# Kernel tuning notes

Hardware: AMD Instinct MI355X
Metric: run time of the kernel (lower is better)

The kernel has to match this reference:

```python
import jax, jax.numpy as jnp
import numpy as np

WIN = (4, 4, 4)   # (wd, wh, ww), window seq len s = 64
HEADS = 4


def setup_inputs() -> dict:
    key = jax.random.key(0)
    k1, k2, k3 = jax.random.split(key, 3)
    B, D, H, W, C = 1, 32, 64, 128, 96
    x = jax.random.normal(k1, (B, D, H, W, C), dtype=jnp.float32)
    # weights stored in (in, out) layout; math identical to torch Linear (x @ W.T)
    w_qkv = jax.random.normal(k2, (C, 3 * C), dtype=jnp.float32) * (C ** -0.5)
    w_proj = jax.random.normal(k3, (C, C), dtype=jnp.float32) * (C ** -0.5)
    b_proj = jnp.zeros((C,), dtype=jnp.float32)
    return {"x": x, "w_qkv": w_qkv, "w_proj": w_proj, "b_proj": b_proj}


def reference(x, w_qkv, w_proj, b_proj):
    B, D, H, W, C = x.shape
    wd, wh, ww = WIN
    h = HEADS
    ch = C // h
    s = wd * wh * ww
    scale = ch ** -0.5
    n, m, l = D // wd, H // wh, W // ww
    # window partition: [B,D,H,W,C] -> [B,n,m,l,s,C]
    xw = x.reshape(B, n, wd, m, wh, l, ww, C)
    xw = xw.transpose(0, 1, 3, 5, 2, 4, 6, 7).reshape(B, n, m, l, s, C)
    # QKV projection (no bias)
    qkv = xw @ w_qkv                      # [B,n,m,l,s,3C]
    q, k, v = jnp.split(qkv, 3, axis=-1)  # each [B,n,m,l,s,C]

    def to_heads(t):
        return t.reshape(B, n, m, l, s, h, ch).transpose(0, 1, 2, 3, 5, 4, 6)

    q, k, v = to_heads(q), to_heads(k), to_heads(v)  # [B,n,m,l,h,s,ch]
    attn = jnp.einsum('bnmlhsc,bnmlhtc->bnmlhst', q, k) * scale
    attn = jax.nn.softmax(attn, axis=-1)             # [B,n,m,l,h,s,s]
    out = jnp.einsum('bnmlhst,bnmlhtc->bnmlhsc', attn, v)
    # merge heads: [B,n,m,l,h,s,ch] -> [B,n,m,l,s,C]
    out = out.transpose(0, 1, 2, 3, 5, 4, 6).reshape(B, n, m, l, s, C)
    out = out @ w_proj + b_proj
    # window merge back to [B,D,H,W,C]
    out = out.reshape(B, n, m, l, wd, wh, ww, C)
    out = out.transpose(0, 1, 4, 2, 5, 3, 6, 7).reshape(B, D, H, W, C)
    return out
```

## Files before the change

kernel.cpp:

```cpp
#include <hip/hip_runtime.h>
#include <hip/hip_bf16.h>

typedef __attribute__((ext_vector_type(8))) short bf16x8;
typedef __attribute__((ext_vector_type(4))) float f32x4;
typedef __attribute__((ext_vector_type(4))) unsigned short u16x4;
typedef __attribute__((ext_vector_type(4))) unsigned int u32x4;
typedef __attribute__((ext_vector_type(2))) unsigned int u32x2;

#define MFMA16(a, b, c) __builtin_amdgcn_mfma_f32_16x16x32_bf16((a), (b), (c), 0, 0, 0)

#define WQT_ELEMS 27648
#define WPT_ELEMS 9216

__device__ __forceinline__ unsigned short cvt_bf(float f) {
    __hip_bfloat16 h = __float2bfloat16(f);
    return *reinterpret_cast<unsigned short*>(&h);
}
__device__ __forceinline__ unsigned pack2bf(float a, float b) {
    return (unsigned)cvt_bf(a) | ((unsigned)cvt_bf(b) << 16);
}

__global__ void wconv_kernel(const float* __restrict__ wqkv,
                             const float* __restrict__ wproj,
                             unsigned short* __restrict__ wsT) {
    int o = blockIdx.x * 256 + threadIdx.x;
    if (o < WQT_ELEMS) {
        int j = o / 96, c = o % 96;
        float w = wqkv[c * 288 + j];
        if (j < 96) w *= 0.2944889313f;
        wsT[o] = cvt_bf(w);
    } else if (o < WQT_ELEMS + WPT_ELEMS) {
        int o2 = o - WQT_ELEMS;
        int j = o2 / 96, c = o2 % 96;
        wsT[o] = cvt_bf(wproj[c * 96 + j]);
    }
}

__device__ __forceinline__ int xq_addr(int t, int c) {
    return ((c >> 5) << 12) + ((t >> 1) << 7)
         + ((((t & 1) << 6) + ((c & 31) << 1)) ^ (((t >> 1) & 7) << 4));
}

#define LOADW(m, W0, W1, W2) do {                                              \
    const unsigned short* _wp = wsT + ((m) * 16 + p) * 96 + qg * 8;            \
    W0 = *reinterpret_cast<const bf16x8*>(_wp);                                \
    W1 = *reinterpret_cast<const bf16x8*>(_wp + 32);                           \
    W2 = *reinterpret_cast<const bf16x8*>(_wp + 64);                           \
} while (0)

#define MFMA_T(W0, W1, W2)                                                     \
    f32x4 ac0 = fzero, ac1 = fzero, ac2 = fzero, ac3 = fzero;                  \
    ac0 = MFMA16(W0, a00, ac0); ac1 = MFMA16(W0, a10, ac1);                    \
    ac2 = MFMA16(W0, a20, ac2); ac3 = MFMA16(W0, a30, ac3);                    \
    ac0 = MFMA16(W1, a01, ac0); ac1 = MFMA16(W1, a11, ac1);                    \
    ac2 = MFMA16(W1, a21, ac2); ac3 = MFMA16(W1, a31, ac3);                    \
    ac0 = MFMA16(W2, a02, ac0); ac1 = MFMA16(W2, a12, ac1);                    \
    ac2 = MFMA16(W2, a22, ac2); ac3 = MFMA16(W2, a32, ac3);

#define DO_Q(m, W0, W1, W2) do {                                               \
    MFMA_T(W0, W1, W2)                                                         \
    int ch = (m) * 16 + 4 * qg;                                                \
    *reinterpret_cast<u32x2*>(xq + xq_addr(p,      ch)) = (u32x2){pack2bf(ac0[0],ac0[1]), pack2bf(ac0[2],ac0[3])}; \
    *reinterpret_cast<u32x2*>(xq + xq_addr(16 + p, ch)) = (u32x2){pack2bf(ac1[0],ac1[1]), pack2bf(ac1[2],ac1[3])}; \
    *reinterpret_cast<u32x2*>(xq + xq_addr(32 + p, ch)) = (u32x2){pack2bf(ac2[0],ac2[1]), pack2bf(ac2[2],ac2[3])}; \
    *reinterpret_cast<u32x2*>(xq + xq_addr(48 + p, ch)) = (u32x2){pack2bf(ac3[0],ac3[1]), pack2bf(ac3[2],ac3[3])}; \
} while (0)

#define DO_K(m, W0, W1, W2) do {                                               \
    MFMA_T(W0, W1, W2)                                                         \
    int jk = ((m) - 6) * 16 + 4 * qg;                                          \
    int cb = jk * 2 + (jk / 24) * 16;                                          \
    int sw = (p & 7) << 4;                                                     \
    *reinterpret_cast<u32x2*>(ksb + (p)      * 256 + (cb ^ sw)) = (u32x2){pack2bf(ac0[0],ac0[1]), pack2bf(ac0[2],ac0[3])}; \
    *reinterpret_cast<u32x2*>(ksb + (16 + p) * 256 + (cb ^ sw)) = (u32x2){pack2bf(ac1[0],ac1[1]), pack2bf(ac1[2],ac1[3])}; \
    *reinterpret_cast<u32x2*>(ksb + (32 + p) * 256 + (cb ^ sw)) = (u32x2){pack2bf(ac2[0],ac2[1]), pack2bf(ac2[2],ac2[3])}; \
    *reinterpret_cast<u32x2*>(ksb + (48 + p) * 256 + (cb ^ sw)) = (u32x2){pack2bf(ac3[0],ac3[1]), pack2bf(ac3[2],ac3[3])}; \
} while (0)

#define STV1(JV, A, T2) do {                                                   \
    int _r0 = (JV);                                                            \
    *reinterpret_cast<unsigned short*>(vtb + (_r0)     * 128 + ((T2) ^ (((_r0)     & 7) << 4))) = cvt_bf(A[0]); \
    *reinterpret_cast<unsigned short*>(vtb + (_r0 + 1) * 128 + ((T2) ^ (((_r0 + 1) & 7) << 4))) = cvt_bf(A[1]); \
    *reinterpret_cast<unsigned short*>(vtb + (_r0 + 2) * 128 + ((T2) ^ (((_r0 + 2) & 7) << 4))) = cvt_bf(A[2]); \
    *reinterpret_cast<unsigned short*>(vtb + (_r0 + 3) * 128 + ((T2) ^ (((_r0 + 3) & 7) << 4))) = cvt_bf(A[3]); \
} while (0)

#define DO_V(m, W0, W1, W2) do {                                               \
    MFMA_T(W0, W1, W2)                                                         \
    int jv = ((m) - 12) * 16 + 4 * qg;                                         \
    STV1(jv, ac0, (p) * 2);                                                    \
    STV1(jv, ac1, (16 + p) * 2);                                               \
    STV1(jv, ac2, (32 + p) * 2);                                               \
    STV1(jv, ac3, (48 + p) * 2);                                               \
} while (0)

#define LOADWP(m, W0, W1, W2) do {                                             \
    const unsigned short* _wp = wpT + ((m) * 16 + p) * 96 + qg * 8;            \
    W0 = *reinterpret_cast<const bf16x8*>(_wp);                                \
    W1 = *reinterpret_cast<const bf16x8*>(_wp + 32);                           \
    W2 = *reinterpret_cast<const bf16x8*>(_wp + 64);                           \
} while (0)

#define PROJ(m, W0, W1, W2) do {                                               \
    f32x4 acc = fzero;                                                         \
    acc = MFMA16(W0, o0, acc);                                                 \
    acc = MFMA16(W1, o1, acc);                                                 \
    acc = MFMA16(W2, o2, acc);                                                 \
    float4 bb = *reinterpret_cast<const float4*>(bproj + (m) * 16 + 4 * qg);   \
    f32x4 r;                                                                   \
    r[0] = acc[0] + bb.x; r[1] = acc[1] + bb.y;                                \
    r[2] = acc[2] + bb.z; r[3] = acc[3] + bb.w;                                \
    *reinterpret_cast<f32x4*>(fbuf + (wv * 16 + p) * 100 + (m) * 16 + 4 * qg) = r; \
} while (0)

__global__ __launch_bounds__(256, 3)
void winattn_kernel(const float* __restrict__ x,
                    const unsigned short* __restrict__ wsT,
                    const float* __restrict__ bproj,
                    float* __restrict__ out) {
    __shared__ __align__(16) char LDS[40960];
    char* xq  = LDS;
    char* ksb = LDS + 12288;
    char* vtb = LDS + 28672;
    float* fbuf = reinterpret_cast<float*>(LDS + 12288);

    const int tid = threadIdx.x;
    const int lane = tid & 63;
    const int wv = tid >> 6;
    const int p  = lane & 15;
    const int qg = lane >> 4;

    const int iw  = blockIdx.x;
    const int l_i = iw & 31;
    const int m_i = (iw >> 5) & 15;
    const int n_i = iw >> 9;

    const f32x4 fzero = {0.f, 0.f, 0.f, 0.f};

    bf16x8 wA0, wA1, wA2, wB0, wB1, wB2;
    const int tb0 = (wv < 2) ? wv * 5 : 10 + (wv - 2) * 4;
    LOADW(tb0, wA0, wA1, wA2);

    #pragma unroll
    for (int it = 0; it < 6; ++it) {
        int slot = tid + it * 256;
        int t = slot / 24, cq = slot % 24;
        int td = t >> 4, th = (t >> 2) & 3, tw = t & 3;
        int off = (((n_i * 4 + td) * 64 + (m_i * 4 + th)) * 128 + (l_i * 4 + tw)) * 96 + cq * 4;
        float4 v4 = *reinterpret_cast<const float4*>(x + off);
        u16x4 h;
        h[0] = cvt_bf(v4.x); h[1] = cvt_bf(v4.y); h[2] = cvt_bf(v4.z); h[3] = cvt_bf(v4.w);
        *reinterpret_cast<u16x4*>(xq + xq_addr(t, cq * 4)) = h;
    }
    {
        int t = tid >> 2, hd = tid & 3;
        bf16x8 z = {0, 0, 0, 0, 0, 0, 0, 0};
        int cb = hd * 64 + 48;
        *reinterpret_cast<bf16x8*>(ksb + t * 256 + (cb ^ ((t & 7) << 4))) = z;
    }
    __syncthreads();

    bf16x8 a00, a01, a02, a10, a11, a12, a20, a21, a22, a30, a31, a32;
    {
        const char* xb = xq;
        a00 = *reinterpret_cast<const bf16x8*>(xb + xq_addr(p,      qg * 8));
        a01 = *reinterpret_cast<const bf16x8*>(xb + xq_addr(p,      32 + qg * 8));
        a02 = *reinterpret_cast<const bf16x8*>(xb + xq_addr(p,      64 + qg * 8));
        a10 = *reinterpret_cast<const bf16x8*>(xb + xq_addr(16 + p, qg * 8));
        a11 = *reinterpret_cast<const bf16x8*>(xb + xq_addr(16 + p, 32 + qg * 8));
        a12 = *reinterpret_cast<const bf16x8*>(xb + xq_addr(16 + p, 64 + qg * 8));
        a20 = *reinterpret_cast<const bf16x8*>(xb + xq_addr(32 + p, qg * 8));
        a21 = *reinterpret_cast<const bf16x8*>(xb + xq_addr(32 + p, 32 + qg * 8));
        a22 = *reinterpret_cast<const bf16x8*>(xb + xq_addr(32 + p, 64 + qg * 8));
        a30 = *reinterpret_cast<const bf16x8*>(xb + xq_addr(48 + p, qg * 8));
        a31 = *reinterpret_cast<const bf16x8*>(xb + xq_addr(48 + p, 32 + qg * 8));
        a32 = *reinterpret_cast<const bf16x8*>(xb + xq_addr(48 + p, 64 + qg * 8));
    }
    __syncthreads();

    if (wv == 0) {
        LOADW(1, wB0, wB1, wB2); DO_Q(0, wA0, wA1, wA2);
        LOADW(2, wA0, wA1, wA2); DO_Q(1, wB0, wB1, wB2);
        LOADW(3, wB0, wB1, wB2); DO_Q(2, wA0, wA1, wA2);
        LOADW(4, wA0, wA1, wA2); DO_Q(3, wB0, wB1, wB2);
        DO_Q(4, wA0, wA1, wA2);
    } else if (wv == 1) {
        LOADW(6, wB0, wB1, wB2); DO_Q(5, wA0, wA1, wA2);
        LOADW(7, wA0, wA1, wA2); DO_K(6, wB0, wB1, wB2);
        LOADW(8, wB0, wB1, wB2); DO_K(7, wA0, wA1, wA2);
        LOADW(9, wA0, wA1, wA2); DO_K(8, wB0, wB1, wB2);
        DO_K(9, wA0, wA1, wA2);
    } else if (wv == 2) {
        LOADW(11, wB0, wB1, wB2); DO_K(10, wA0, wA1, wA2);
        LOADW(12, wA0, wA1, wA2); DO_K(11, wB0, wB1, wB2);
        LOADW(13, wB0, wB1, wB2); DO_V(12, wA0, wA1, wA2);
        DO_V(13, wB0, wB1, wB2);
    } else {
        LOADW(15, wB0, wB1, wB2); DO_V(14, wA0, wA1, wA2);
        LOADW(16, wA0, wA1, wA2); DO_V(15, wB0, wB1, wB2);
        LOADW(17, wB0, wB1, wB2); DO_V(16, wA0, wA1, wA2);
        DO_V(17, wB0, wB1, wB2);
    }
    __syncthreads();

    #pragma unroll 1
    for (int hd = 0; hd < 4; ++hd) {
        bf16x8 aqh = *reinterpret_cast<const bf16x8*>(xq + xq_addr(wv * 16 + p, hd * 24 + qg * 8));
        f32x4 sacc[4];
        #pragma unroll
        for (int nt = 0; nt < 4; ++nt) {
            int t = nt * 16 + p;
            bf16x8 ak = *reinterpret_cast<const bf16x8*>(ksb + t * 256 + ((hd * 64 + qg * 16) ^ ((t & 7) << 4)));
            sacc[nt] = MFMA16(ak, aqh, fzero);
        }
        float mm = sacc[0][0];
        #pragma unroll
        for (int nt = 0; nt < 4; ++nt)
            #pragma unroll
            for (int rg = 0; rg < 4; ++rg)
                mm = fmaxf(mm, sacc[nt][rg]);
        mm = fmaxf(mm, __shfl_xor(mm, 16));
        mm = fmaxf(mm, __shfl_xor(mm, 32));
        float pw[4][4];
        float sum = 0.f;
        #pragma unroll
        for (int nt = 0; nt < 4; ++nt)
            #pragma unroll
            for (int rg = 0; rg < 4; ++rg) {
                float e = exp2f(sacc[nt][rg] - mm);
                pw[nt][rg] = e;
                sum += e;
            }
        sum += __shfl_xor(sum, 16);
        sum += __shfl_xor(sum, 32);
        float inv = 1.0f / sum;
        unsigned pk[4][2];
        #pragma unroll
        for (int nt = 0; nt < 4; ++nt) {
            pk[nt][0] = pack2bf(pw[nt][0] * inv, pw[nt][1] * inv);
            pk[nt][1] = pack2bf(pw[nt][2] * inv, pw[nt][3] * inv);
        }
        u32x4 pa0, pa1;
        #pragma unroll
        for (int d = 0; d < 4; ++d) {
            int src = ((qg & 1) * 2 + (d >> 1)) * 16 + p;
            int lo0 = __shfl((int)pk[0][d & 1], src);
            int hi0 = __shfl((int)pk[1][d & 1], src);
            int lo1 = __shfl((int)pk[2][d & 1], src);
            int hi1 = __shfl((int)pk[3][d & 1], src);
            pa0[d] = (qg < 2) ? (unsigned)lo0 : (unsigned)hi0;
            pa1[d] = (qg < 2) ? (unsigned)lo1 : (unsigned)hi1;
        }
        bf16x8 pA0 = __builtin_bit_cast(bf16x8, pa0);
        bf16x8 pA1 = __builtin_bit_cast(bf16x8, pa1);
        f32x4 oacc[2] = {fzero, fzero};
        #pragma unroll
        for (int n2 = 0; n2 < 2; ++n2) {
            int vr = hd * 24 + n2 * 16 + p;
            vr = vr > 95 ? 95 : vr;
            int rb = vr * 128, sw = (vr & 7) << 4;
            bf16x8 av0 = *reinterpret_cast<const bf16x8*>(vtb + rb + ((qg * 16) ^ sw));
            bf16x8 av1 = *reinterpret_cast<const bf16x8*>(vtb + rb + ((64 + qg * 16) ^ sw));
            oacc[n2] = MFMA16(av0, pA0, oacc[n2]);
            oacc[n2] = MFMA16(av1, pA1, oacc[n2]);
        }
        {
            u32x2 w0 = { pack2bf(oacc[0][0], oacc[0][1]), pack2bf(oacc[0][2], oacc[0][3]) };
            *reinterpret_cast<u32x2*>(xq + xq_addr(wv * 16 + p, hd * 24 + 4 * qg)) = w0;
            if (qg < 2) {
                u32x2 w1 = { pack2bf(oacc[1][0], oacc[1][1]), pack2bf(oacc[1][2], oacc[1][3]) };
                *reinterpret_cast<u32x2*>(xq + xq_addr(wv * 16 + p, hd * 24 + 16 + 4 * qg)) = w1;
            }
        }
    }

    bf16x8 o0, o1, o2;
    o0 = *reinterpret_cast<const bf16x8*>(xq + xq_addr(wv * 16 + p, qg * 8));
    o1 = *reinterpret_cast<const bf16x8*>(xq + xq_addr(wv * 16 + p, 32 + qg * 8));
    o2 = *reinterpret_cast<const bf16x8*>(xq + xq_addr(wv * 16 + p, 64 + qg * 8));
    __syncthreads();

    const unsigned short* wpT = wsT + WQT_ELEMS;
    LOADWP(0, wA0, wA1, wA2);
    LOADWP(1, wB0, wB1, wB2); PROJ(0, wA0, wA1, wA2);
    LOADWP(2, wA0, wA1, wA2); PROJ(1, wB0, wB1, wB2);
    LOADWP(3, wB0, wB1, wB2); PROJ(2, wA0, wA1, wA2);
    LOADWP(4, wA0, wA1, wA2); PROJ(3, wB0, wB1, wB2);
    LOADWP(5, wB0, wB1, wB2); PROJ(4, wA0, wA1, wA2);
    PROJ(5, wB0, wB1, wB2);
    __syncthreads();

    #pragma unroll
    for (int it = 0; it < 6; ++it) {
        int slot = tid + it * 256;
        int t = slot / 24, cq = slot % 24;
        int td = t >> 4, th = (t >> 2) & 3, tw = t & 3;
        int off = (((n_i * 4 + td) * 64 + (m_i * 4 + th)) * 128 + (l_i * 4 + tw)) * 96 + cq * 4;
        float4 v4 = *reinterpret_cast<const float4*>(fbuf + t * 100 + cq * 4);
        *reinterpret_cast<float4*>(out + off) = v4;
    }
}

extern "C" void kernel_launch(void* const* d_in, const int* in_sizes, int n_in,
                              void* d_out, int out_size, void* d_ws, size_t ws_size,
                              hipStream_t stream) {
    const float* x     = (const float*)d_in[0];
    const float* wqkv  = (const float*)d_in[1];
    const float* wproj = (const float*)d_in[2];
    const float* bproj = (const float*)d_in[3];
    float* out = (float*)d_out;
    unsigned short* wsT = (unsigned short*)d_ws;

    wconv_kernel<<<dim3((WQT_ELEMS + WPT_ELEMS) / 256), dim3(256), 0, stream>>>(wqkv, wproj, wsT);
    winattn_kernel<<<dim3(4096), dim3(256), 0, stream>>>(x, wsT, bproj, out);
}
```

Before: 80.16 us.

## Store K in compact xq layout, shrink LDS, raise occupancy to four blocks

K is now written into the same compact 96-channel swizzled layout as Q instead of a padded 256-byte-per-row layout with zeroed head padding. Padding lanes are handled by zeroing the Q operand for qg==3 and clamping the read column, so the per-block zero-fill pass goes away. fbuf is moved to alias the start of LDS. Together these cut LDS from 40 KB to 36 KB, and launch bounds go from 3 to 4 blocks per CU to allow more resident waves. The risks are register pressure under the tighter launch bound and a correctness hazard if fbuf overwrites Q or K before every wave has finished reading them.

```diff
diff --git a/kernel.cpp b/kernel.cpp
--- a/kernel.cpp
+++ b/kernel.cpp
@@ -57,25 +57,16 @@
     ac0 = MFMA16(W2, a02, ac0); ac1 = MFMA16(W2, a12, ac1);                    \
     ac2 = MFMA16(W2, a22, ac2); ac3 = MFMA16(W2, a32, ac3);
 
-#define DO_Q(m, W0, W1, W2) do {                                               \
+#define DO_QK(DST, ch, W0, W1, W2) do {                                        \
     MFMA_T(W0, W1, W2)                                                         \
-    int ch = (m) * 16 + 4 * qg;                                                \
-    *reinterpret_cast<u32x2*>(xq + xq_addr(p,      ch)) = (u32x2){pack2bf(ac0[0],ac0[1]), pack2bf(ac0[2],ac0[3])}; \
-    *reinterpret_cast<u32x2*>(xq + xq_addr(16 + p, ch)) = (u32x2){pack2bf(ac1[0],ac1[1]), pack2bf(ac1[2],ac1[3])}; \
-    *reinterpret_cast<u32x2*>(xq + xq_addr(32 + p, ch)) = (u32x2){pack2bf(ac2[0],ac2[1]), pack2bf(ac2[2],ac2[3])}; \
-    *reinterpret_cast<u32x2*>(xq + xq_addr(48 + p, ch)) = (u32x2){pack2bf(ac3[0],ac3[1]), pack2bf(ac3[2],ac3[3])}; \
-} while (0)
-
-#define DO_K(m, W0, W1, W2) do {                                               \
-    MFMA_T(W0, W1, W2)                                                         \
-    int jk = ((m) - 6) * 16 + 4 * qg;                                          \
-    int cb = jk * 2 + (jk / 24) * 16;                                          \
-    int sw = (p & 7) << 4;                                                     \
-    *reinterpret_cast<u32x2*>(ksb + (p)      * 256 + (cb ^ sw)) = (u32x2){pack2bf(ac0[0],ac0[1]), pack2bf(ac0[2],ac0[3])}; \
-    *reinterpret_cast<u32x2*>(ksb + (16 + p) * 256 + (cb ^ sw)) = (u32x2){pack2bf(ac1[0],ac1[1]), pack2bf(ac1[2],ac1[3])}; \
-    *reinterpret_cast<u32x2*>(ksb + (32 + p) * 256 + (cb ^ sw)) = (u32x2){pack2bf(ac2[0],ac2[1]), pack2bf(ac2[2],ac2[3])}; \
-    *reinterpret_cast<u32x2*>(ksb + (48 + p) * 256 + (cb ^ sw)) = (u32x2){pack2bf(ac3[0],ac3[1]), pack2bf(ac3[2],ac3[3])}; \
-} while (0)
+    *reinterpret_cast<u32x2*>((DST) + xq_addr(p,      (ch))) = (u32x2){pack2bf(ac0[0],ac0[1]), pack2bf(ac0[2],ac0[3])}; \
+    *reinterpret_cast<u32x2*>((DST) + xq_addr(16 + p, (ch))) = (u32x2){pack2bf(ac1[0],ac1[1]), pack2bf(ac1[2],ac1[3])}; \
+    *reinterpret_cast<u32x2*>((DST) + xq_addr(32 + p, (ch))) = (u32x2){pack2bf(ac2[0],ac2[1]), pack2bf(ac2[2],ac2[3])}; \
+    *reinterpret_cast<u32x2*>((DST) + xq_addr(48 + p, (ch))) = (u32x2){pack2bf(ac3[0],ac3[1]), pack2bf(ac3[2],ac3[3])}; \
+} while (0)
+
+#define DO_Q(m, W0, W1, W2) DO_QK(xq, (m) * 16 + 4 * qg, W0, W1, W2)
+#define DO_K(m, W0, W1, W2) DO_QK(kb, ((m) - 6) * 16 + 4 * qg, W0, W1, W2)
 
 #define STV1(JV, A, T2) do {                                                   \
     int _r0 = (JV);                                                            \
@@ -113,16 +104,16 @@
     *reinterpret_cast<f32x4*>(fbuf + (wv * 16 + p) * 100 + (m) * 16 + 4 * qg) = r; \
 } while (0)
 
-__global__ __launch_bounds__(256, 3)
+__global__ __launch_bounds__(256, 4)
 void winattn_kernel(const float* __restrict__ x,
                     const unsigned short* __restrict__ wsT,
                     const float* __restrict__ bproj,
                     float* __restrict__ out) {
-    __shared__ __align__(16) char LDS[40960];
+    __shared__ __align__(16) char LDS[36864];
     char* xq  = LDS;
-    char* ksb = LDS + 12288;
-    char* vtb = LDS + 28672;
-    float* fbuf = reinterpret_cast<float*>(LDS + 12288);
+    char* kb  = LDS + 12288;
+    char* vtb = LDS + 24576;
+    float* fbuf = reinterpret_cast<float*>(LDS);
 
     const int tid = threadIdx.x;
     const int lane = tid & 63;
@@ -136,6 +127,7 @@
     const int n_i = iw >> 9;
 
     const f32x4 fzero = {0.f, 0.f, 0.f, 0.f};
+    const bf16x8 zero8 = {0, 0, 0, 0, 0, 0, 0, 0};
 
     bf16x8 wA0, wA1, wA2, wB0, wB1, wB2;
     const int tb0 = (wv < 2) ? wv * 5 : 10 + (wv - 2) * 4;
@@ -151,12 +143,6 @@
         u16x4 h;
         h[0] = cvt_bf(v4.x); h[1] = cvt_bf(v4.y); h[2] = cvt_bf(v4.z); h[3] = cvt_bf(v4.w);
         *reinterpret_cast<u16x4*>(xq + xq_addr(t, cq * 4)) = h;
-    }
-    {
-        int t = tid >> 2, hd = tid & 3;
-        bf16x8 z = {0, 0, 0, 0, 0, 0, 0, 0};
-        int cb = hd * 64 + 48;
-        *reinterpret_cast<bf16x8*>(ksb + t * 256 + (cb ^ ((t & 7) << 4))) = z;
     }
     __syncthreads();
 
@@ -205,12 +191,14 @@
 
     #pragma unroll 1
     for (int hd = 0; hd < 4; ++hd) {
-        bf16x8 aqh = *reinterpret_cast<const bf16x8*>(xq + xq_addr(wv * 16 + p, hd * 24 + qg * 8));
+        int qc = hd * 24 + qg * 8;
+        qc = qc > 88 ? 88 : qc;
+        bf16x8 aq_raw = *reinterpret_cast<const bf16x8*>(xq + xq_addr(wv * 16 + p, qc));
+        bf16x8 aqh = (qg == 3) ? zero8 : aq_raw;
         f32x4 sacc[4];
         #pragma unroll
         for (int nt = 0; nt < 4; ++nt) {
-            int t = nt * 16 + p;
-            bf16x8 ak = *reinterpret_cast<const bf16x8*>(ksb + t * 256 + ((hd * 64 + qg * 16) ^ ((t & 7) << 4)));
+            bf16x8 ak = *reinterpret_cast<const bf16x8*>(kb + xq_addr(nt * 16 + p, qc));
             sacc[nt] = MFMA16(ak, aqh, fzero);
         }
         float mm = sacc[0][0];
```

After: 96.31 us. 20.1% more time.
